# Performance work log

Hardware: AMD Instinct MI355X
Metric: run time of the kernel (lower is better)

## Reference

```python
import jax, jax.numpy as jnp
import numpy as np

N_HEAD, D_K, D_V, D_MODEL, D_O = 8, 64, 64, 512, 512
B, S = 2, 4096

def setup_inputs() -> dict:
    key = jax.random.key(0)
    ks = jax.random.split(key, 11)
    s = 1.0 / np.sqrt(D_MODEL)
    so = 1.0 / np.sqrt(N_HEAD * D_V)
    return {
        'q': jax.random.normal(ks[0], (B, S, D_MODEL), jnp.float32),
        'k': jax.random.normal(ks[1], (B, S, D_MODEL), jnp.float32),
        'v': jax.random.normal(ks[2], (B, S, D_MODEL), jnp.float32),
        'Wq': jax.random.uniform(ks[3], (D_MODEL, N_HEAD * D_K), jnp.float32, -s, s),
        'bq': jax.random.uniform(ks[4], (N_HEAD * D_K,), jnp.float32, -s, s),
        'Wk': jax.random.uniform(ks[5], (D_MODEL, N_HEAD * D_K), jnp.float32, -s, s),
        'bk': jax.random.uniform(ks[6], (N_HEAD * D_K,), jnp.float32, -s, s),
        'Wv': jax.random.uniform(ks[7], (D_MODEL, N_HEAD * D_V), jnp.float32, -s, s),
        'bv': jax.random.uniform(ks[8], (N_HEAD * D_V,), jnp.float32, -s, s),
        'Wo': jax.random.uniform(ks[9], (N_HEAD * D_V, D_O), jnp.float32, -so, so),
        'bo': jax.random.uniform(ks[10], (D_O,), jnp.float32, -so, so),
    }

def reference(q, k, v, Wq, bq, Wk, bk, Wv, bv, Wo, bo):
    b, nq, _ = q.shape
    nk = k.shape[1]
    scale = jnp.asarray(np.power(D_K, 0.5), q.dtype)
    # project and split heads: [b, s, h, d]
    qh = (q @ Wq + bq).reshape(b, nq, N_HEAD, D_K)
    kh = (k @ Wk + bk).reshape(b, nk, N_HEAD, D_K)
    vh = (v @ Wv + bv).reshape(b, nk, N_HEAD, D_V)
    # scaled dot-product attention (full score matrix, as in original)
    scores = jnp.einsum('bqhd,bkhd->bhqk', qh, kh) / scale
    attn = jax.nn.softmax(scores, axis=-1)
    out = jnp.einsum('bhqk,bkhd->bqhd', attn, vh)
    # concat heads (head-major over d_v, matching the original view) and output proj
    out = out.reshape(b, nq, N_HEAD * D_V)
    return out @ Wo + bo
```

## Files before the change

### kernel.cpp

```cpp
#include <hip/hip_runtime.h>
#include <hip/hip_bf16.h>

#define NHEAD 8
#define DK_ 64
#define DM_ 512
#define S_LEN 4096
#define NTOK 8192

typedef __bf16 bf16x8 __attribute__((ext_vector_type(8)));
typedef float f32x4 __attribute__((ext_vector_type(4)));
typedef float f32x16 __attribute__((ext_vector_type(16)));
typedef unsigned int uint4v __attribute__((ext_vector_type(4)));

__device__ __forceinline__ unsigned short f2bf(float f) {
    union { float f; unsigned u; } x; x.f = f;
    unsigned u = x.u;
    u += 0x7FFFu + ((u >> 16) & 1u);
    return (unsigned short)(u >> 16);
}

#if __has_builtin(__builtin_amdgcn_cvt_pk_bf16_f32)
__device__ __forceinline__ unsigned int pkbf(float a, float b) {
    auto r = __builtin_amdgcn_cvt_pk_bf16_f32(a, b);
    unsigned int u; __builtin_memcpy(&u, &r, 4); return u;
}
#else
__device__ __forceinline__ unsigned int pkbf(float a, float b) {
    return (unsigned)f2bf(a) | ((unsigned)f2bf(b) << 16);
}
#endif

#if __has_builtin(__builtin_amdgcn_exp2f)
#define EXP2F(x) __builtin_amdgcn_exp2f(x)
#else
#define EXP2F(x) exp2f(x)
#endif

#if __has_builtin(__builtin_amdgcn_permlane32_swap)
__device__ __forceinline__ void pl32swap(unsigned int& a, unsigned int& b) {
    auto r = __builtin_amdgcn_permlane32_swap(a, b, false, false);
    a = r[0]; b = r[1];
}
#else
__device__ __forceinline__ void pl32swap(unsigned int& a, unsigned int& b) {
    int lane = threadIdx.x & 63;
    unsigned int ax = __shfl_xor((int)a, 32, 64);
    unsigned int bx = __shfl_xor((int)b, 32, 64);
    unsigned int na = (lane < 32) ? a : bx;
    unsigned int nb = (lane < 32) ? ax : b;
    a = na; b = nb;
}
#endif

#define GLOAD_LDS16(gptr, ldsbase) \
    __builtin_amdgcn_global_load_lds((const __attribute__((address_space(1))) unsigned int*)(gptr), \
                                     (__attribute__((address_space(3))) unsigned int*)(ldsbase), 16, 0, 0)

__global__ __launch_bounds__(256) void xcvt(const float* __restrict__ q, const float* __restrict__ k,
                                            const float* __restrict__ v, unsigned short* __restrict__ Xbf) {
    int z = blockIdx.y;
    const float* X = (z == 0) ? q : (z == 1) ? k : v;
    size_t off = (size_t)blockIdx.x * 1024 + threadIdx.x * 4;
    float4 val = *(const float4*)&X[off];
    uint2 o; o.x = pkbf(val.x, val.y); o.y = pkbf(val.z, val.w);
    *(uint2*)&Xbf[(size_t)z * NTOK * DM_ + off] = o;
}

__global__ __launch_bounds__(256) void wtrans(const float* __restrict__ Wq, const float* __restrict__ Wk,
                                              const float* __restrict__ Wv, const float* __restrict__ Wo,
                                              unsigned short* __restrict__ Wt) {
    int z = blockIdx.z;
    const float* W = (z == 0) ? Wq : (z == 1) ? Wk : (z == 2) ? Wv : Wo;
    unsigned short* out = Wt + (size_t)z * DM_ * DM_;
    __shared__ float t[64][65];
    int bn = blockIdx.x * 64, bk = blockIdx.y * 64;
    int tid = threadIdx.x;
    int r0 = tid >> 4, c4 = (tid & 15) * 4;
#pragma unroll
    for (int i = 0; i < 4; i++) {
        int r = r0 + i * 16;
        float4 v = *(const float4*)&W[(size_t)(bk + r) * DM_ + bn + c4];
        t[r][c4] = v.x; t[r][c4 + 1] = v.y; t[r][c4 + 2] = v.z; t[r][c4 + 3] = v.w;
    }
    __syncthreads();
    int n0 = tid >> 4, k4 = (tid & 15) * 4;
#pragma unroll
    for (int i = 0; i < 4; i++) {
        int n = n0 + i * 16;
        ushort4 o;
        o.x = f2bf(t[k4 + 0][n]); o.y = f2bf(t[k4 + 1][n]);
        o.z = f2bf(t[k4 + 2][n]); o.w = f2bf(t[k4 + 3][n]);
        *(ushort4*)&out[(size_t)(bn + n) * DM_ + bk + k4] = o;
    }
}

__device__ __forceinline__ void proj_epilogue(int z, f32x4 (&acc)[4][4], const float* bias,
                                              unsigned short* out, float scale,
                                              int m0, int n0, int mb, int nb, int ln, int qd) {
    float bvv[4];
#pragma unroll
    for (int nt = 0; nt < 4; nt++) bvv[nt] = bias[n0 + nb + nt * 16 + ln];
#pragma unroll
    for (int mt = 0; mt < 4; mt++) {
        int mrow0 = m0 + mb + mt * 16 + qd * 4;
        int b = mrow0 >> 12, s = mrow0 & 4095;
#pragma unroll
        for (int nt = 0; nt < 4; nt++) {
            int ncol = n0 + nb + nt * 16 + ln;
            int h = ncol >> 6, d = ncol & 63;
            if (z == 2) {
                uint2 o;
                o.x = pkbf((acc[mt][nt][0] + bvv[nt]) * scale, (acc[mt][nt][1] + bvv[nt]) * scale);
                o.y = pkbf((acc[mt][nt][2] + bvv[nt]) * scale, (acc[mt][nt][3] + bvv[nt]) * scale);
                *(uint2*)&out[((size_t)(b * NHEAD + h) * DK_ + d) * S_LEN + s] = o;
            } else {
#pragma unroll
                for (int r = 0; r < 4; r++)
                    out[((size_t)(b * NHEAD + h) * S_LEN + (s + r)) * DK_ + d] =
                        f2bf((acc[mt][nt][r] + bvv[nt]) * scale);
            }
        }
    }
}

__global__ __launch_bounds__(256, 3) void qkv_bf(const unsigned short* __restrict__ Xbf,
                                                 const unsigned short* __restrict__ Wt,
                                                 const float* __restrict__ bq, const float* __restrict__ bk,
                                                 const float* __restrict__ bv,
                                                 unsigned short* __restrict__ Qh, unsigned short* __restrict__ Kh,
                                                 unsigned short* __restrict__ VhT) {
    int z = blockIdx.z;
    const unsigned short* X = Xbf + (size_t)z * NTOK * DM_;
    const unsigned short* W = Wt + (size_t)z * DM_ * DM_;
    const float* bias = (z == 0) ? bq : (z == 1) ? bk : bv;
    unsigned short* out = (z == 0) ? Qh : (z == 1) ? Kh : VhT;
    float scale = (z == 0) ? 0.125f * 1.44269504f : 1.0f;

    __shared__ unsigned short As[128 * 40];
    __shared__ unsigned short Bs[128 * 40];
    int tid = threadIdx.x;
    int n0 = blockIdx.x * 128, m0 = blockIdx.y * 128;
    int w = tid >> 6, lane = tid & 63;
    int ln = lane & 15, qd = lane >> 4;
    int mb = (w >> 1) * 64, nb = (w & 1) * 64;

    f32x4 acc[4][4];
#pragma unroll
    for (int i = 0; i < 4; i++)
#pragma unroll
        for (int j = 0; j < 4; j++) { f32x4 zz = {0.f, 0.f, 0.f, 0.f}; acc[i][j] = zz; }

    for (int kk = 0; kk < DM_; kk += 32) {
        __syncthreads();
#pragma unroll
        for (int i = 0; i < 2; i++) {
            int idx = i * 256 + tid;
            int row = idx >> 2, k8 = (idx & 3) * 8;
            uint4 va = *(const uint4*)&X[(size_t)(m0 + row) * DM_ + kk + k8];
            *(uint4*)&As[row * 40 + k8] = va;
            uint4 vb = *(const uint4*)&W[(size_t)(n0 + row) * DM_ + kk + k8];
            *(uint4*)&Bs[row * 40 + k8] = vb;
        }
        __syncthreads();
        bf16x8 af[4], bf[4];
#pragma unroll
        for (int mt = 0; mt < 4; mt++) af[mt] = *(const bf16x8*)&As[(mb + mt * 16 + ln) * 40 + qd * 8];
#pragma unroll
        for (int nt = 0; nt < 4; nt++) bf[nt] = *(const bf16x8*)&Bs[(nb + nt * 16 + ln) * 40 + qd * 8];
#pragma unroll
        for (int mt = 0; mt < 4; mt++)
#pragma unroll
            for (int nt = 0; nt < 4; nt++)
                acc[mt][nt] = __builtin_amdgcn_mfma_f32_16x16x32_bf16(af[mt], bf[nt], acc[mt][nt], 0, 0, 0);
    }
    proj_epilogue(z, acc, bias, out, scale, m0, n0, mb, nb, ln, qd);
}

__global__ __launch_bounds__(256, 3) void qkv_proj(const float* __restrict__ xq, const float* __restrict__ xk,
                                                   const float* __restrict__ xv, const unsigned short* __restrict__ Wt,
                                                   const float* __restrict__ bq, const float* __restrict__ bk,
                                                   const float* __restrict__ bv,
                                                   unsigned short* __restrict__ Qh, unsigned short* __restrict__ Kh,
                                                   unsigned short* __restrict__ VhT) {
    int z = blockIdx.z;
    const float* X = (z == 0) ? xq : (z == 1) ? xk : xv;
    const unsigned short* W = Wt + (size_t)z * DM_ * DM_;
    const float* bias = (z == 0) ? bq : (z == 1) ? bk : bv;
    unsigned short* out = (z == 0) ? Qh : (z == 1) ? Kh : VhT;
    float scale = (z == 0) ? 0.125f * 1.44269504f : 1.0f;

    __shared__ unsigned short As[128 * 40];
    __shared__ unsigned short Bs[128 * 40];
    int tid = threadIdx.x;
    int n0 = blockIdx.x * 128, m0 = blockIdx.y * 128;
    int w = tid >> 6, lane = tid & 63;
    int ln = lane & 15, qd = lane >> 4;
    int mb = (w >> 1) * 64, nb = (w & 1) * 64;

    f32x4 acc[4][4];
#pragma unroll
    for (int i = 0; i < 4; i++)
#pragma unroll
        for (int j = 0; j < 4; j++) { f32x4 zz = {0.f, 0.f, 0.f, 0.f}; acc[i][j] = zz; }

    for (int kk = 0; kk < DM_; kk += 32) {
        __syncthreads();
#pragma unroll
        for (int i = 0; i < 4; i++) {
            int idx = i * 256 + tid;
            int row = idx >> 3, k4 = (idx & 7) * 4;
            float4 v = *(const float4*)&X[(size_t)(m0 + row) * DM_ + kk + k4];
            uint2 o; o.x = pkbf(v.x, v.y); o.y = pkbf(v.z, v.w);
            *(uint2*)&As[row * 40 + k4] = o;
        }
#pragma unroll
        for (int i = 0; i < 2; i++) {
            int idx = i * 256 + tid;
            int row = idx >> 2, k8 = (idx & 3) * 8;
            uint4 v = *(const uint4*)&W[(size_t)(n0 + row) * DM_ + kk + k8];
            *(uint4*)&Bs[row * 40 + k8] = v;
        }
        __syncthreads();
        bf16x8 af[4], bf[4];
#pragma unroll
        for (int mt = 0; mt < 4; mt++) af[mt] = *(const bf16x8*)&As[(mb + mt * 16 + ln) * 40 + qd * 8];
#pragma unroll
        for (int nt = 0; nt < 4; nt++) bf[nt] = *(const bf16x8*)&Bs[(nb + nt * 16 + ln) * 40 + qd * 8];
#pragma unroll
        for (int mt = 0; mt < 4; mt++)
#pragma unroll
            for (int nt = 0; nt < 4; nt++)
                acc[mt][nt] = __builtin_amdgcn_mfma_f32_16x16x32_bf16(af[mt], bf[nt], acc[mt][nt], 0, 0, 0);
    }
    proj_epilogue(z, acc, bias, out, scale, m0, n0, mb, nb, ln, qd);
}

__global__ __launch_bounds__(256, 2) void flash_attn(const unsigned short* __restrict__ Qh,
                                                     const unsigned short* __restrict__ Kh,
                                                     const unsigned short* __restrict__ VhT,
                                                     unsigned short* __restrict__ Ao) {
    __shared__ unsigned short Ks[2][64 * 64];
    __shared__ unsigned short Vs[2][64 * 64];
    int i = blockIdx.x;
    int bh = (i & 7) + 8 * ((i >> 3) & 1);
    int qb = i >> 4;
    int tid = threadIdx.x;
    int w = tid >> 6, lane = tid & 63;
    int ln = lane & 31, hf = lane >> 5;
    int swz = ln & 7;
    int q0 = qb * 128 + w * 32;
    const unsigned short* Qp = Qh + (size_t)bh * S_LEN * DK_;
    const unsigned short* Kp = Kh + (size_t)bh * S_LEN * DK_;
    const unsigned short* Vp = VhT + (size_t)bh * DK_ * S_LEN;

    int sr = lane >> 3;
    int sc = (lane & 7) ^ sr;
    const unsigned short* ksrc = Kp + (size_t)(w * 16 + sr) * DK_ + sc * 8;
    const unsigned short* vsrc = Vp + (size_t)(w * 16 + sr) * S_LEN + sc * 8;

    bf16x8 qf[4];
#pragma unroll
    for (int s = 0; s < 4; s++)
        qf[s] = *(const bf16x8*)&Qp[(size_t)(q0 + ln) * DK_ + s * 16 + hf * 8];

    f32x16 oacc[2];
    { f32x16 z = {0.f}; oacc[0] = z; oacc[1] = z; }
    float lsum = 0.f;

    GLOAD_LDS16(ksrc, &Ks[0][w * 1024]);
    GLOAD_LDS16(ksrc + (size_t)8 * DK_, &Ks[0][w * 1024 + 512]);
    GLOAD_LDS16(vsrc, &Vs[0][w * 1024]);
    GLOAD_LDS16(vsrc + (size_t)8 * S_LEN, &Vs[0][w * 1024 + 512]);

    int p = 0;
    for (int ks = 0; ks < S_LEN; ks += 64, p ^= 1) {
        __syncthreads();
        if (ks + 64 < S_LEN) {
            const unsigned short* kn = ksrc + (size_t)(ks + 64) * DK_;
            const unsigned short* vn = vsrc + (ks + 64);
            GLOAD_LDS16(kn, &Ks[p ^ 1][w * 1024]);
            GLOAD_LDS16(kn + (size_t)8 * DK_, &Ks[p ^ 1][w * 1024 + 512]);
            GLOAD_LDS16(vn, &Vs[p ^ 1][w * 1024]);
            GLOAD_LDS16(vn + (size_t)8 * S_LEN, &Vs[p ^ 1][w * 1024 + 512]);
        }
        const unsigned short* KsT = &Ks[p][0];
        const unsigned short* VsT = &Vs[p][0];

#pragma unroll
        for (int kb = 0; kb < 2; kb++) {
            f32x16 st = {0.f};
#pragma unroll
            for (int s = 0; s < 4; s++) {
                bf16x8 kf = *(const bf16x8*)&KsT[(kb * 32 + ln) * 64 + ((2 * s + hf) ^ swz) * 8];
                st = __builtin_amdgcn_mfma_f32_32x32x16_bf16(kf, qf[s], st, 0, 0, 0);
            }
            float e[16];
#pragma unroll
            for (int r = 0; r < 16; r++) e[r] = EXP2F(st[r]);
            lsum += ((e[0] + e[1]) + (e[2] + e[3])) + ((e[4] + e[5]) + (e[6] + e[7]))
                  + ((e[8] + e[9]) + (e[10] + e[11])) + ((e[12] + e[13]) + (e[14] + e[15]));
            unsigned int g[8];
#pragma unroll
            for (int gi = 0; gi < 8; gi++) g[gi] = pkbf(e[2 * gi], e[2 * gi + 1]);
            pl32swap(g[0], g[2]); pl32swap(g[1], g[3]);
            pl32swap(g[4], g[6]); pl32swap(g[5], g[7]);
            bf16x8 b0, b1;
            { uint4v t = {g[0], g[1], g[2], g[3]}; __builtin_memcpy(&b0, &t, 16); }
            { uint4v t = {g[4], g[5], g[6], g[7]}; __builtin_memcpy(&b1, &t, 16); }
#pragma unroll
            for (int dt = 0; dt < 2; dt++) {
                int s0 = kb * 2;
                bf16x8 vf0 = *(const bf16x8*)&VsT[(dt * 32 + ln) * 64 + ((2 * s0 + hf) ^ swz) * 8];
                bf16x8 vf1 = *(const bf16x8*)&VsT[(dt * 32 + ln) * 64 + ((2 * s0 + 2 + hf) ^ swz) * 8];
                oacc[dt] = __builtin_amdgcn_mfma_f32_32x32x16_bf16(vf0, b0, oacc[dt], 0, 0, 0);
                oacc[dt] = __builtin_amdgcn_mfma_f32_32x32x16_bf16(vf1, b1, oacc[dt], 0, 0, 0);
            }
        }
    }

    float ltot = lsum + __shfl_xor(lsum, 32, 64);
    float inv = 1.0f / ltot;

    int bb = bh >> 3, hh = bh & 7;
    int token = bb * S_LEN + q0 + ln;
#pragma unroll
    for (int dt = 0; dt < 2; dt++)
#pragma unroll
        for (int gi = 0; gi < 8; gi++) {
            int d = dt * 32 + 2 * (gi & 1) + 8 * (gi >> 1) + 4 * hf;
            unsigned int o = pkbf(oacc[dt][2 * gi] * inv, oacc[dt][2 * gi + 1] * inv);
            *(unsigned int*)&Ao[(size_t)token * DM_ + hh * DK_ + d] = o;
        }
}

__global__ __launch_bounds__(256, 2) void flash_attn_sp2(const unsigned short* __restrict__ Qh,
                                                         const unsigned short* __restrict__ Kh,
                                                         const unsigned short* __restrict__ VhT,
                                                         float* __restrict__ Opart,
                                                         float* __restrict__ lpart) {
    __shared__ unsigned short Ks[2][64 * 64];
    __shared__ unsigned short Vs[2][64 * 64];
    int i = blockIdx.x;
    int bh = (i & 7) + 8 * ((i >> 3) & 1);
    int qb = (i >> 4) & 15;
    int sp = i >> 8;
    int ks0 = sp * (S_LEN / 2);
    int ks1 = ks0 + (S_LEN / 2);
    int tid = threadIdx.x;
    int w = tid >> 6, lane = tid & 63;
    int ln = lane & 31, hf = lane >> 5;
    int swz = ln & 7;
    int q0 = qb * 256 + w * 64;
    const unsigned short* Qp = Qh + (size_t)bh * S_LEN * DK_;
    const unsigned short* Kp = Kh + (size_t)bh * S_LEN * DK_;
    const unsigned short* Vp = VhT + (size_t)bh * DK_ * S_LEN;

    int sr = lane >> 3;
    int sc = (lane & 7) ^ sr;
    const unsigned short* ksrc = Kp + (size_t)(w * 16 + sr) * DK_ + sc * 8;
    const unsigned short* vsrc = Vp + (size_t)(w * 16 + sr) * S_LEN + sc * 8;

    bf16x8 qfA[4], qfB[4];
#pragma unroll
    for (int s = 0; s < 4; s++) {
        qfA[s] = *(const bf16x8*)&Qp[(size_t)(q0 + ln) * DK_ + s * 16 + hf * 8];
        qfB[s] = *(const bf16x8*)&Qp[(size_t)(q0 + 32 + ln) * DK_ + s * 16 + hf * 8];
    }

    f32x16 oaccA[2], oaccB[2];
    { f32x16 z = {0.f}; oaccA[0] = z; oaccA[1] = z; oaccB[0] = z; oaccB[1] = z; }
    float lsumA = 0.f, lsumB = 0.f;

    GLOAD_LDS16(ksrc + (size_t)ks0 * DK_, &Ks[0][w * 1024]);
    GLOAD_LDS16(ksrc + (size_t)(ks0 + 8) * DK_, &Ks[0][w * 1024 + 512]);
    GLOAD_LDS16(vsrc + ks0, &Vs[0][w * 1024]);
    GLOAD_LDS16(vsrc + ks0 + (size_t)8 * S_LEN, &Vs[0][w * 1024 + 512]);

    int p = 0;
    for (int ks = ks0; ks < ks1; ks += 64, p ^= 1) {
        __syncthreads();
        if (ks + 64 < ks1) {
            const unsigned short* kn = ksrc + (size_t)(ks + 64) * DK_;
            const unsigned short* vn = vsrc + (ks + 64);
            GLOAD_LDS16(kn, &Ks[p ^ 1][w * 1024]);
            GLOAD_LDS16(kn + (size_t)8 * DK_, &Ks[p ^ 1][w * 1024 + 512]);
            GLOAD_LDS16(vn, &Vs[p ^ 1][w * 1024]);
            GLOAD_LDS16(vn + (size_t)8 * S_LEN, &Vs[p ^ 1][w * 1024 + 512]);
        }
        const unsigned short* KsT = &Ks[p][0];
        const unsigned short* VsT = &Vs[p][0];

#pragma unroll
        for (int kb = 0; kb < 2; kb++) {
            f32x16 stA = {0.f}, stB = {0.f};
#pragma unroll
            for (int s = 0; s < 4; s++) {
                bf16x8 kf = *(const bf16x8*)&KsT[(kb * 32 + ln) * 64 + ((2 * s + hf) ^ swz) * 8];
                stA = __builtin_amdgcn_mfma_f32_32x32x16_bf16(kf, qfA[s], stA, 0, 0, 0);
                stB = __builtin_amdgcn_mfma_f32_32x32x16_bf16(kf, qfB[s], stB, 0, 0, 0);
            }
            bf16x8 b0A, b1A, b0B, b1B;
            {
                float e[16];
#pragma unroll
                for (int r = 0; r < 16; r++) e[r] = EXP2F(stA[r]);
                lsumA += ((e[0] + e[1]) + (e[2] + e[3])) + ((e[4] + e[5]) + (e[6] + e[7]))
                       + ((e[8] + e[9]) + (e[10] + e[11])) + ((e[12] + e[13]) + (e[14] + e[15]));
                unsigned int g[8];
#pragma unroll
                for (int gi = 0; gi < 8; gi++) g[gi] = pkbf(e[2 * gi], e[2 * gi + 1]);
                pl32swap(g[0], g[2]); pl32swap(g[1], g[3]);
                pl32swap(g[4], g[6]); pl32swap(g[5], g[7]);
                { uint4v t = {g[0], g[1], g[2], g[3]}; __builtin_memcpy(&b0A, &t, 16); }
                { uint4v t = {g[4], g[5], g[6], g[7]}; __builtin_memcpy(&b1A, &t, 16); }
            }
            {
                float e[16];
#pragma unroll
                for (int r = 0; r < 16; r++) e[r] = EXP2F(stB[r]);
                lsumB += ((e[0] + e[1]) + (e[2] + e[3])) + ((e[4] + e[5]) + (e[6] + e[7]))
                       + ((e[8] + e[9]) + (e[10] + e[11])) + ((e[12] + e[13]) + (e[14] + e[15]));
                unsigned int g[8];
#pragma unroll
                for (int gi = 0; gi < 8; gi++) g[gi] = pkbf(e[2 * gi], e[2 * gi + 1]);
                pl32swap(g[0], g[2]); pl32swap(g[1], g[3]);
                pl32swap(g[4], g[6]); pl32swap(g[5], g[7]);
                { uint4v t = {g[0], g[1], g[2], g[3]}; __builtin_memcpy(&b0B, &t, 16); }
                { uint4v t = {g[4], g[5], g[6], g[7]}; __builtin_memcpy(&b1B, &t, 16); }
            }
#pragma unroll
            for (int dt = 0; dt < 2; dt++) {
                int s0 = kb * 2;
                bf16x8 vf0 = *(const bf16x8*)&VsT[(dt * 32 + ln) * 64 + ((2 * s0 + hf) ^ swz) * 8];
                bf16x8 vf1 = *(const bf16x8*)&VsT[(dt * 32 + ln) * 64 + ((2 * s0 + 2 + hf) ^ swz) * 8];
                oaccA[dt] = __builtin_amdgcn_mfma_f32_32x32x16_bf16(vf0, b0A, oaccA[dt], 0, 0, 0);
                oaccA[dt] = __builtin_amdgcn_mfma_f32_32x32x16_bf16(vf1, b1A, oaccA[dt], 0, 0, 0);
                oaccB[dt] = __builtin_amdgcn_mfma_f32_32x32x16_bf16(vf0, b0B, oaccB[dt], 0, 0, 0);
                oaccB[dt] = __builtin_amdgcn_mfma_f32_32x32x16_bf16(vf1, b1B, oaccB[dt], 0, 0, 0);
            }
        }
    }

    float ltotA = lsumA + __shfl_xor(lsumA, 32, 64);
    float ltotB = lsumB + __shfl_xor(lsumB, 32, 64);
    if (hf == 0) {
        lpart[(size_t)sp * (16 * S_LEN) + (size_t)bh * S_LEN + q0 + ln] = ltotA;
        lpart[(size_t)sp * (16 * S_LEN) + (size_t)bh * S_LEN + q0 + 32 + ln] = ltotB;
    }

    int bb = bh >> 3, hh = bh & 7;
    float* op = Opart + (size_t)sp * NTOK * DM_;
    int tokenA = bb * S_LEN + q0 + ln;
    int tokenB = tokenA + 32;
#pragma unroll
    for (int dt = 0; dt < 2; dt++)
#pragma unroll
        for (int gi = 0; gi < 8; gi++) {
            int d = dt * 32 + 2 * (gi & 1) + 8 * (gi >> 1) + 4 * hf;
            float2 oa; oa.x = oaccA[dt][2 * gi]; oa.y = oaccA[dt][2 * gi + 1];
            *(float2*)&op[(size_t)tokenA * DM_ + hh * DK_ + d] = oa;
            float2 ob; ob.x = oaccB[dt][2 * gi]; ob.y = oaccB[dt][2 * gi + 1];
            *(float2*)&op[(size_t)tokenB * DM_ + hh * DK_ + d] = ob;
        }
}

__global__ __launch_bounds__(256) void merge_split(const float* __restrict__ Opart,
                                                   const float* __restrict__ lpart,
                                                   unsigned short* __restrict__ Ao) {
    size_t e = ((size_t)blockIdx.x * 256 + threadIdx.x) * 4;
    int token = (int)(e >> 9);
    int c = (int)(e & 511);
    int hh = c >> 6;
    int bb = token >> 12, s = token & 4095;
    size_t li = (size_t)(bb * NHEAD + hh) * S_LEN + s;
    float l0 = lpart[li];
    float l1 = lpart[(size_t)16 * S_LEN + li];
    float inv = 1.0f / (l0 + l1);
    float4 a = *(const float4*)&Opart[e];
    float4 b = *(const float4*)&Opart[(size_t)NTOK * DM_ + e];
    uint2 o;
    o.x = pkbf((a.x + b.x) * inv, (a.y + b.y) * inv);
    o.y = pkbf((a.z + b.z) * inv, (a.w + b.w) * inv);
    *(uint2*)&Ao[e] = o;
}

__global__ __launch_bounds__(256) void out_gemm(const unsigned short* __restrict__ A,
                                                const unsigned short* __restrict__ Wt,
                                                const float* __restrict__ bias, float* __restrict__ out) {
    __shared__ unsigned short As[128 * 40];
    __shared__ unsigned short Bs[128 * 40];
    int tid = threadIdx.x;
    int n0 = blockIdx.x * 128, m0 = blockIdx.y * 128;
    int w = tid >> 6, lane = tid & 63;
    int ln = lane & 15, qd = lane >> 4;
    int mb = (w >> 1) * 64, nb = (w & 1) * 64;

    f32x4 acc[4][4];
#pragma unroll
    for (int i = 0; i < 4; i++)
#pragma unroll
        for (int j = 0; j < 4; j++) { f32x4 z = {0.f, 0.f, 0.f, 0.f}; acc[i][j] = z; }

    for (int kk = 0; kk < DM_; kk += 32) {
        __syncthreads();
#pragma unroll
        for (int i = 0; i < 2; i++) {
            int idx = i * 256 + tid;
            int row = idx >> 2, k8 = (idx & 3) * 8;
            uint4 va = *(const uint4*)&A[(size_t)(m0 + row) * DM_ + kk + k8];
            *(uint4*)&As[row * 40 + k8] = va;
            uint4 vb = *(const uint4*)&Wt[(size_t)(n0 + row) * DM_ + kk + k8];
            *(uint4*)&Bs[row * 40 + k8] = vb;
        }
        __syncthreads();
        bf16x8 af[4], bf[4];
#pragma unroll
        for (int mt = 0; mt < 4; mt++) af[mt] = *(const bf16x8*)&As[(mb + mt * 16 + ln) * 40 + qd * 8];
#pragma unroll
        for (int nt = 0; nt < 4; nt++) bf[nt] = *(const bf16x8*)&Bs[(nb + nt * 16 + ln) * 40 + qd * 8];
#pragma unroll
        for (int mt = 0; mt < 4; mt++)
#pragma unroll
            for (int nt = 0; nt < 4; nt++)
                acc[mt][nt] = __builtin_amdgcn_mfma_f32_16x16x32_bf16(af[mt], bf[nt], acc[mt][nt], 0, 0, 0);
    }

    float bv[4];
#pragma unroll
    for (int nt = 0; nt < 4; nt++) bv[nt] = bias[n0 + nb + nt * 16 + ln];
#pragma unroll
    for (int mt = 0; mt < 4; mt++) {
        int mrow0 = m0 + mb + mt * 16 + qd * 4;
#pragma unroll
        for (int nt = 0; nt < 4; nt++) {
            int ncol = n0 + nb + nt * 16 + ln;
#pragma unroll
            for (int r = 0; r < 4; r++)
                out[(size_t)(mrow0 + r) * DM_ + ncol] = acc[mt][nt][r] + bv[nt];
        }
    }
}

extern "C" void kernel_launch(void* const* d_in, const int* in_sizes, int n_in,
                              void* d_out, int out_size, void* d_ws, size_t ws_size,
                              hipStream_t stream) {
    const float* q  = (const float*)d_in[0];
    const float* k  = (const float*)d_in[1];
    const float* v  = (const float*)d_in[2];
    const float* Wq = (const float*)d_in[3];
    const float* bq = (const float*)d_in[4];
    const float* Wk = (const float*)d_in[5];
    const float* bk = (const float*)d_in[6];
    const float* Wv = (const float*)d_in[7];
    const float* bv = (const float*)d_in[8];
    const float* Wo = (const float*)d_in[9];
    const float* bo = (const float*)d_in[10];
    float* out = (float*)d_out;

    unsigned short* Wt  = (unsigned short*)d_ws;
    unsigned short* Qh  = Wt + (size_t)4 * DM_ * DM_;
    unsigned short* Kh  = Qh + (size_t)NTOK * DM_;
    unsigned short* VhT = Kh + (size_t)NTOK * DM_;
    unsigned short* tail = VhT + (size_t)NTOK * DM_;

    float* Opart = (float*)tail;
    float* lpart = Opart + (size_t)2 * NTOK * DM_;
    unsigned short* Ao_sp = (unsigned short*)(lpart + (size_t)2 * 16 * S_LEN);

    size_t head_b  = ((size_t)4 * DM_ * DM_ + (size_t)3 * NTOK * DM_) * 2;
    size_t need_sp = head_b + (size_t)2 * NTOK * DM_ * 4 + (size_t)2 * 16 * S_LEN * 4 + (size_t)NTOK * DM_ * 2;
    size_t need_bf = ((size_t)4 * DM_ * DM_ + (size_t)6 * NTOK * DM_) * 2;

    wtrans<<<dim3(8, 8, 4), 256, 0, stream>>>(Wq, Wk, Wv, Wo, Wt);
    if (ws_size >= need_sp) {
        unsigned short* Xbf = tail;
        xcvt<<<dim3(4096, 3), 256, 0, stream>>>(q, k, v, Xbf);
        qkv_bf<<<dim3(4, 64, 3), 256, 0, stream>>>(Xbf, Wt, bq, bk, bv, Qh, Kh, VhT);
        flash_attn_sp2<<<dim3(512), 256, 0, stream>>>(Qh, Kh, VhT, Opart, lpart);
        merge_split<<<dim3(4096), 256, 0, stream>>>(Opart, lpart, Ao_sp);
        out_gemm<<<dim3(4, 64), 256, 0, stream>>>(Ao_sp, Wt + (size_t)3 * DM_ * DM_, bo, out);
    } else if (ws_size >= need_bf) {
        unsigned short* Xbf = tail;
        unsigned short* Ao = tail;
        xcvt<<<dim3(4096, 3), 256, 0, stream>>>(q, k, v, Xbf);
        qkv_bf<<<dim3(4, 64, 3), 256, 0, stream>>>(Xbf, Wt, bq, bk, bv, Qh, Kh, VhT);
        flash_attn<<<dim3(512), 256, 0, stream>>>(Qh, Kh, VhT, Ao);
        out_gemm<<<dim3(4, 64), 256, 0, stream>>>(Ao, Wt + (size_t)3 * DM_ * DM_, bo, out);
    } else {
        unsigned short* Ao = tail;
        qkv_proj<<<dim3(4, 64, 3), 256, 0, stream>>>(q, k, v, Wt, bq, bk, bv, Qh, Kh, VhT);
        flash_attn<<<dim3(512), 256, 0, stream>>>(Qh, Kh, VhT, Ao);
        out_gemm<<<dim3(4, 64), 256, 0, stream>>>(Ao, Wt + (size_t)3 * DM_ * DM_, bo, out);
    }
}
```

Baseline: 251.0 us.

## Split attention keys four ways, raise occupancy, and prioritize MFMA waves

The default path now splits the key range into four parts instead of two, so 1024 blocks run instead of 512. Each split writes fp32 partial outputs and row sums, and a templated merge kernel adds them. Launch bounds rise to 4 blocks per CU, and s_setprio brackets the MFMA sections so waves doing matrix work get issue priority. A fallback path with a two-way split and 32 query rows per wave is added. The cost is extra fp32 partial traffic: four partial buffers are written and read in the merge.

```diff
diff --git a/kernel.cpp b/kernel.cpp
--- a/kernel.cpp
+++ b/kernel.cpp
@@ -333,7 +333,111 @@
         }
 }
 
-__global__ __launch_bounds__(256, 2) void flash_attn_sp2(const unsigned short* __restrict__ Qh,
+__global__ __launch_bounds__(256, 4) void flash_attn_sp(const unsigned short* __restrict__ Qh,
+                                                        const unsigned short* __restrict__ Kh,
+                                                        const unsigned short* __restrict__ VhT,
+                                                        float* __restrict__ Opart,
+                                                        float* __restrict__ lpart) {
+    __shared__ unsigned short Ks[2][64 * 64];
+    __shared__ unsigned short Vs[2][64 * 64];
+    int i = blockIdx.x;
+    int bh = (i & 7) + 8 * ((i >> 3) & 1);
+    int qb = (i >> 4) & 31;
+    int sp = i >> 9;
+    int ks0 = sp * (S_LEN / 2);
+    int ks1 = ks0 + (S_LEN / 2);
+    int tid = threadIdx.x;
+    int w = tid >> 6, lane = tid & 63;
+    int ln = lane & 31, hf = lane >> 5;
+    int swz = ln & 7;
+    int q0 = qb * 128 + w * 32;
+    const unsigned short* Qp = Qh + (size_t)bh * S_LEN * DK_;
+    const unsigned short* Kp = Kh + (size_t)bh * S_LEN * DK_;
+    const unsigned short* Vp = VhT + (size_t)bh * DK_ * S_LEN;
+
+    int sr = lane >> 3;
+    int sc = (lane & 7) ^ sr;
+    const unsigned short* ksrc = Kp + (size_t)(w * 16 + sr) * DK_ + sc * 8;
+    const unsigned short* vsrc = Vp + (size_t)(w * 16 + sr) * S_LEN + sc * 8;
+
+    bf16x8 qf[4];
+#pragma unroll
+    for (int s = 0; s < 4; s++)
+        qf[s] = *(const bf16x8*)&Qp[(size_t)(q0 + ln) * DK_ + s * 16 + hf * 8];
+
+    f32x16 oacc[2];
+    { f32x16 z = {0.f}; oacc[0] = z; oacc[1] = z; }
+    float lsum = 0.f;
+
+    GLOAD_LDS16(ksrc + (size_t)ks0 * DK_, &Ks[0][w * 1024]);
+    GLOAD_LDS16(ksrc + (size_t)(ks0 + 8) * DK_, &Ks[0][w * 1024 + 512]);
+    GLOAD_LDS16(vsrc + ks0, &Vs[0][w * 1024]);
+    GLOAD_LDS16(vsrc + ks0 + (size_t)8 * S_LEN, &Vs[0][w * 1024 + 512]);
+
+    int p = 0;
+    for (int ks = ks0; ks < ks1; ks += 64, p ^= 1) {
+        __syncthreads();
+        if (ks + 64 < ks1) {
+            const unsigned short* kn = ksrc + (size_t)(ks + 64) * DK_;
+            const unsigned short* vn = vsrc + (ks + 64);
+            GLOAD_LDS16(kn, &Ks[p ^ 1][w * 1024]);
+            GLOAD_LDS16(kn + (size_t)8 * DK_, &Ks[p ^ 1][w * 1024 + 512]);
+            GLOAD_LDS16(vn, &Vs[p ^ 1][w * 1024]);
+            GLOAD_LDS16(vn + (size_t)8 * S_LEN, &Vs[p ^ 1][w * 1024 + 512]);
+        }
+        const unsigned short* KsT = &Ks[p][0];
+        const unsigned short* VsT = &Vs[p][0];
+
+#pragma unroll
+        for (int kb = 0; kb < 2; kb++) {
+            f32x16 st = {0.f};
+#pragma unroll
+            for (int s = 0; s < 4; s++) {
+                bf16x8 kf = *(const bf16x8*)&KsT[(kb * 32 + ln) * 64 + ((2 * s + hf) ^ swz) * 8];
+                st = __builtin_amdgcn_mfma_f32_32x32x16_bf16(kf, qf[s], st, 0, 0, 0);
+            }
+            float e[16];
+#pragma unroll
+            for (int r = 0; r < 16; r++) e[r] = EXP2F(st[r]);
+            lsum += ((e[0] + e[1]) + (e[2] + e[3])) + ((e[4] + e[5]) + (e[6] + e[7]))
+                  + ((e[8] + e[9]) + (e[10] + e[11])) + ((e[12] + e[13]) + (e[14] + e[15]));
+            unsigned int g[8];
+#pragma unroll
+            for (int gi = 0; gi < 8; gi++) g[gi] = pkbf(e[2 * gi], e[2 * gi + 1]);
+            pl32swap(g[0], g[2]); pl32swap(g[1], g[3]);
+            pl32swap(g[4], g[6]); pl32swap(g[5], g[7]);
+            bf16x8 b0, b1;
+            { uint4v t = {g[0], g[1], g[2], g[3]}; __builtin_memcpy(&b0, &t, 16); }
+            { uint4v t = {g[4], g[5], g[6], g[7]}; __builtin_memcpy(&b1, &t, 16); }
+#pragma unroll
+            for (int dt = 0; dt < 2; dt++) {
+                int s0 = kb * 2;
+                bf16x8 vf0 = *(const bf16x8*)&VsT[(dt * 32 + ln) * 64 + ((2 * s0 + hf) ^ swz) * 8];
+                bf16x8 vf1 = *(const bf16x8*)&VsT[(dt * 32 + ln) * 64 + ((2 * s0 + 2 + hf) ^ swz) * 8];
+                oacc[dt] = __builtin_amdgcn_mfma_f32_32x32x16_bf16(vf0, b0, oacc[dt], 0, 0, 0);
+                oacc[dt] = __builtin_amdgcn_mfma_f32_32x32x16_bf16(vf1, b1, oacc[dt], 0, 0, 0);
+            }
+        }
+    }
+
+    float ltot = lsum + __shfl_xor(lsum, 32, 64);
+    if (hf == 0)
+        lpart[(size_t)sp * (16 * S_LEN) + (size_t)bh * S_LEN + q0 + ln] = ltot;
+
+    int bb = bh >> 3, hh = bh & 7;
+    int token = bb * S_LEN + q0 + ln;
+    float* op = Opart + (size_t)sp * NTOK * DM_;
+#pragma unroll
+    for (int dt = 0; dt < 2; dt++)
+#pragma unroll
+        for (int gi = 0; gi < 8; gi++) {
+            int d = dt * 32 + 2 * (gi & 1) + 8 * (gi >> 1) + 4 * hf;
+            float2 o; o.x = oacc[dt][2 * gi]; o.y = oacc[dt][2 * gi + 1];
+            *(float2*)&op[(size_t)token * DM_ + hh * DK_ + d] = o;
+        }
+}
+
+__global__ __launch_bounds__(256, 4) void flash_attn_sp4(const unsigned short* __restrict__ Qh,
                                                          const unsigned short* __restrict__ Kh,
                                                          const unsigned short* __restrict__ VhT,
                                                          float* __restrict__ Opart,
@@ -341,11 +445,11 @@
     __shared__ unsigned short Ks[2][64 * 64];
     __shared__ unsigned short Vs[2][64 * 64];
     int i = blockIdx.x;
-    int bh = (i & 7) + 8 * ((i >> 3) & 1);
+    int bh = i & 15;
     int qb = (i >> 4) & 15;
     int sp = i >> 8;
-    int ks0 = sp * (S_LEN / 2);
-    int ks1 = ks0 + (S_LEN / 2);
+    int ks0 = sp * (S_LEN / 4);
+    int ks1 = ks0 + (S_LEN / 4);
     int tid = threadIdx.x;
     int w = tid >> 6, lane = tid & 63;
     int ln = lane & 31, hf = lane >> 5;
@@ -393,12 +497,14 @@
 #pragma unroll
         for (int kb = 0; kb < 2; kb++) {
             f32x16 stA = {0.f}, stB = {0.f};
+            __builtin_amdgcn_s_setprio(1);
 #pragma unroll
             for (int s = 0; s < 4; s++) {
                 bf16x8 kf = *(const bf16x8*)&KsT[(kb * 32 + ln) * 64 + ((2 * s + hf) ^ swz) * 8];
                 stA = __builtin_amdgcn_mfma_f32_32x32x16_bf16(kf, qfA[s], stA, 0, 0, 0);
                 stB = __builtin_amdgcn_mfma_f32_32x32x16_bf16(kf, qfB[s], stB, 0, 0, 0);
             }
+            __builtin_amdgcn_s_setprio(0);
             bf16x8 b0A, b1A, b0B, b1B;
             {
                 float e[16];
@@ -428,6 +534,7 @@
                 { uint4v t = {g[0], g[1], g[2], g[3]}; __builtin_memcpy(&b0B, &t, 16); }
                 { uint4v t = {g[4], g[5], g[6], g[7]}; __builtin_memcpy(&b1B, &t, 16); }
             }
+            __builtin_amdgcn_s_setprio(1);
 #pragma unroll
             for (int dt = 0; dt < 2; dt++) {
                 int s0 = kb * 2;
@@ -438,6 +545,7 @@
                 oaccB[dt] = __builtin_amdgcn_mfma_f32_32x32x16_bf16(vf0, b0B, oaccB[dt], 0, 0, 0);
                 oaccB[dt] = __builtin_amdgcn_mfma_f32_32x32x16_bf16(vf1, b1B, oaccB[dt], 0, 0, 0);
             }
+            __builtin_amdgcn_s_setprio(0);
         }
     }
 
@@ -464,6 +572,7 @@
         }
 }
 
+template <int NSP>
 __global__ __launch_bounds__(256) void merge_split(const float* __restrict__ Opart,
                                                    const float* __restrict__ lpart,
                                                    unsigned short* __restrict__ Ao) {
@@ -473,14 +582,19 @@
     int hh = c >> 6;
     int bb = token >> 12, s = token & 4095;
     size_t li = (size_t)(bb * NHEAD + hh) * S_LEN + s;
-    float l0 = lpart[li];
-    float l1 = lpart[(size_t)16 * S_LEN + li];
-    float inv = 1.0f / (l0 + l1);
+    float ltot = 0.f;
+#pragma unroll
+    for (int j = 0; j < NSP; j++) ltot += lpart[(size_t)j * (16 * S_LEN) + li];
+    float inv = 1.0f / ltot;
     float4 a = *(const float4*)&Opart[e];
-    float4 b = *(const float4*)&Opart[(size_t)NTOK * DM_ + e];
+#pragma unroll
+    for (int j = 1; j < NSP; j++) {
+        float4 b = *(const float4*)&Opart[(size_t)j * NTOK * DM_ + e];
+        a.x += b.x; a.y += b.y; a.z += b.z; a.w += b.w;
+    }
     uint2 o;
-    o.x = pkbf((a.x + b.x) * inv, (a.y + b.y) * inv);
-    o.y = pkbf((a.z + b.z) * inv, (a.w + b.w) * inv);
+    o.x = pkbf(a.x * inv, a.y * inv);
+    o.y = pkbf(a.z * inv, a.w * inv);
     *(uint2*)&Ao[e] = o;
 }
 
@@ -563,22 +677,37 @@
     unsigned short* VhT = Kh + (size_t)NTOK * DM_;
     unsigned short* tail = VhT + (size_t)NTOK * DM_;
 
-    float* Opart = (float*)tail;
-    float* lpart = Opart + (size_t)2 * NTOK * DM_;
-    unsigned short* Ao_sp = (unsigned short*)(lpart + (size_t)2 * 16 * S_LEN);
-
     size_t head_b  = ((size_t)4 * DM_ * DM_ + (size_t)3 * NTOK * DM_) * 2;
-    size_t need_sp = head_b + (size_t)2 * NTOK * DM_ * 4 + (size_t)2 * 16 * S_LEN * 4 + (size_t)NTOK * DM_ * 2;
-    size_t need_bf = ((size_t)4 * DM_ * DM_ + (size_t)6 * NTOK * DM_) * 2;
+    size_t opart_b4 = (size_t)4 * NTOK * DM_ * 4;
+    size_t lpart_b4 = (size_t)4 * 16 * S_LEN * 4;
+    size_t opart_b2 = (size_t)2 * NTOK * DM_ * 4;
+    size_t lpart_b2 = (size_t)2 * 16 * S_LEN * 4;
+    size_t ao_b     = (size_t)NTOK * DM_ * 2;
+    size_t need_sp4 = head_b + opart_b4 + lpart_b4 + ao_b;
+    size_t need_sp2 = head_b + opart_b2 + lpart_b2 + ao_b;
+    size_t need_bf  = ((size_t)4 * DM_ * DM_ + (size_t)6 * NTOK * DM_) * 2;
 
     wtrans<<<dim3(8, 8, 4), 256, 0, stream>>>(Wq, Wk, Wv, Wo, Wt);
-    if (ws_size >= need_sp) {
+    if (ws_size >= need_sp4) {
+        float* Opart = (float*)tail;
+        float* lpart = Opart + (size_t)4 * NTOK * DM_;
+        unsigned short* Ao = (unsigned short*)(lpart + (size_t)4 * 16 * S_LEN);
         unsigned short* Xbf = tail;
         xcvt<<<dim3(4096, 3), 256, 0, stream>>>(q, k, v, Xbf);
         qkv_bf<<<dim3(4, 64, 3), 256, 0, stream>>>(Xbf, Wt, bq, bk, bv, Qh, Kh, VhT);
-        flash_attn_sp2<<<dim3(512), 256, 0, stream>>>(Qh, Kh, VhT, Opart, lpart);
-        merge_split<<<dim3(4096), 256, 0, stream>>>(Opart, lpart, Ao_sp);
-        out_gemm<<<dim3(4, 64), 256, 0, stream>>>(Ao_sp, Wt + (size_t)3 * DM_ * DM_, bo, out);
+        flash_attn_sp4<<<dim3(1024), 256, 0, stream>>>(Qh, Kh, VhT, Opart, lpart);
+        merge_split<4><<<dim3(4096), 256, 0, stream>>>(Opart, lpart, Ao);
+        out_gemm<<<dim3(4, 64), 256, 0, stream>>>(Ao, Wt + (size_t)3 * DM_ * DM_, bo, out);
+    } else if (ws_size >= need_sp2) {
+        float* Opart = (float*)tail;
+        float* lpart = Opart + (size_t)2 * NTOK * DM_;
+        unsigned short* Ao = (unsigned short*)(lpart + (size_t)2 * 16 * S_LEN);
+        unsigned short* Xbf = tail;
+        xcvt<<<dim3(4096, 3), 256, 0, stream>>>(q, k, v, Xbf);
+        qkv_bf<<<dim3(4, 64, 3), 256, 0, stream>>>(Xbf, Wt, bq, bk, bv, Qh, Kh, VhT);
+        flash_attn_sp<<<dim3(1024), 256, 0, stream>>>(Qh, Kh, VhT, Opart, lpart);
+        merge_split<2><<<dim3(4096), 256, 0, stream>>>(Opart, lpart, Ao);
+        out_gemm<<<dim3(4, 64), 256, 0, stream>>>(Ao, Wt + (size_t)3 * DM_ * DM_, bo, out);
     } else if (ws_size >= need_bf) {
         unsigned short* Xbf = tail;
         unsigned short* Ao = tail;
```

After: 384.5 us. 53.2% more time.
